# Performance work log

Measured on AMD Instinct MI355X. Metric: run time of the kernel, lower is better.

The kernel has to match this reference:

```python
import jax, jax.numpy as jnp
import numpy as np

NUM_HEADS = 8
NUM_POINTS = 4


def _bilinear_sample(value_hw, locs, H, W):
    """grid_sample(mode='bilinear', align_corners=False, padding_mode='zeros').
    value_hw: [B, heads, H*W, hd]; locs: [B, Nq, heads, P, 2] in [0,1].
    Returns [B, Nq, heads, P, hd]."""
    B, Nq, heads, P, _ = locs.shape
    hd = value_hw.shape[-1]
    # torch maps g in [-1,1] -> pixel ((g+1)*size-1)/2; with g = 2*loc-1 this is loc*size - 0.5
    x = locs[..., 0] * W - 0.5
    y = locs[..., 1] * H - 0.5
    x0 = jnp.floor(x); y0 = jnp.floor(y)
    wx = x - x0; wy = y - y0
    ix0 = x0.astype(jnp.int32); iy0 = y0.astype(jnp.int32)
    ix1 = ix0 + 1; iy1 = iy0 + 1

    def gather(iy, ix):
        valid = (ix >= 0) & (ix < W) & (iy >= 0) & (iy < H)
        flat = jnp.clip(iy, 0, H - 1) * W + jnp.clip(ix, 0, W - 1)  # [B,Nq,heads,P]
        flat_t = flat.transpose(0, 2, 1, 3).reshape(B, heads, Nq * P)
        v = jnp.take_along_axis(value_hw, flat_t[..., None], axis=2)  # [B,heads,Nq*P,hd]
        v = v.reshape(B, heads, Nq, P, hd).transpose(0, 2, 1, 3, 4)
        return v * valid[..., None].astype(v.dtype)

    out = (gather(iy0, ix0) * ((1 - wx) * (1 - wy))[..., None]
           + gather(iy0, ix1) * (wx * (1 - wy))[..., None]
           + gather(iy1, ix0) * ((1 - wx) * wy)[..., None]
           + gather(iy1, ix1) * (wx * wy)[..., None])
    return out


def setup_inputs() -> dict:
    key = jax.random.key(0)
    ks = jax.random.split(key, 12)
    B, Nq, C, H, W = 4, 8192, 256, 128, 128
    heads, P = NUM_HEADS, NUM_POINTS
    s = 1.0 / np.sqrt(C)
    return {
        "query": jax.random.normal(ks[0], (B, Nq, C), jnp.float32),
        "reference_points": jax.random.uniform(ks[1], (B, Nq, 2), jnp.float32),
        "value": jax.random.normal(ks[2], (B, H * W, C), jnp.float32),
        "W_off": jax.random.normal(ks[3], (C, heads * P * 2), jnp.float32) * s,
        "b_off": jax.random.normal(ks[4], (heads * P * 2,), jnp.float32) * 0.5,
        "W_attn": jax.random.normal(ks[5], (C, heads * P), jnp.float32) * s,
        "b_attn": jax.random.normal(ks[6], (heads * P,), jnp.float32) * 0.1,
        "W_v": jax.random.normal(ks[7], (C, C), jnp.float32) * s,
        "b_v": jax.random.normal(ks[8], (C,), jnp.float32) * 0.1,
        "W_out": jax.random.normal(ks[9], (C, C), jnp.float32) * s,
        "b_out": jax.random.normal(ks[10], (C,), jnp.float32) * 0.1,
        "H": H,
        "W": W,
    }


def reference(query, reference_points, value, W_off, b_off, W_attn, b_attn,
              W_v, b_v, W_out, b_out, H, W):
    B, Nq, C = query.shape
    heads, P = NUM_HEADS, NUM_POINTS
    hd = C // heads

    offsets = (query @ W_off + b_off).reshape(B, Nq, heads, P, 2)
    attn = jax.nn.softmax((query @ W_attn + b_attn).reshape(B, Nq, heads, P), axis=-1)

    off_x = offsets[..., 0] / float(W) * 0.1
    off_y = offsets[..., 1] / float(H) * 0.1
    locs = reference_points[:, :, None, None, :] + jnp.stack([off_x, off_y], axis=-1)
    locs = jnp.clip(locs, 0.0, 1.0)  # [B,Nq,heads,P,2]

    # value projection -> [B, heads, H*W, hd]
    v = (value @ W_v + b_v).reshape(B, H * W, heads, hd).transpose(0, 2, 1, 3)

    sampled = _bilinear_sample(v, locs, H, W)            # [B,Nq,heads,P,hd]
    agg = jnp.einsum('bnhp,bnhpd->bnhd', attn, sampled)  # weighted sum over points
    out = agg.reshape(B, Nq, C) @ W_out + b_out
    return out
```

## Files before the change

kernel.cpp:

```cpp
#include <hip/hip_runtime.h>
#include <cstdint>

#define NB 4
#define NQ 8192
#define NC 256
#define IH 128
#define IW 128
#define NHW (IH * IW)
#define NHEADS 8
#define NP 4
#define NHD 32

typedef __bf16 bf16x8 __attribute__((ext_vector_type(8)));
typedef float f32x4 __attribute__((ext_vector_type(4)));

union FragCast { uint4 q; bf16x8 v; };

__device__ __forceinline__ unsigned int f2bf(float f) {
    unsigned int u = __float_as_uint(f);
    return (u + 0x7FFFu + ((u >> 16) & 1u)) >> 16;
}
__device__ __forceinline__ float bf2f(unsigned short s) {
    return __uint_as_float(((unsigned int)s) << 16);
}

__global__ __launch_bounds__(256) void k_pack(
    const float* __restrict__ Wv, const float* __restrict__ Wout,
    const float* __restrict__ Woff, const float* __restrict__ Wattn,
    unsigned short* __restrict__ pkv, unsigned short* __restrict__ pko,
    unsigned short* __restrict__ pkq)
{
    const int tid = blockIdx.x * 256 + threadIdx.x;
    if (tid < 4096) {
        const float* src = (tid & 2048) ? Wout : Wv;
        unsigned short* dst = (tid & 2048) ? pko : pkv;
        const int rem = tid & 2047;
        const int kt = rem >> 8, col = rem & 255;
        unsigned short* d = dst + (size_t)(kt * 256 + col) * 32;
        const float* s = src + (size_t)kt * 32 * 256 + col;
#pragma unroll
        for (int j = 0; j < 32; ++j)
            d[j] = (unsigned short)f2bf(s[(size_t)j * 256]);
    } else {
        const int rem = tid - 4096;
        const int kt = rem / 96, col = rem % 96;
        unsigned short* d = pkq + (size_t)(kt * 96 + col) * 32;
        const float* s; int stride;
        if (col < 64) { s = Woff + col; stride = 64; }
        else          { s = Wattn + (col - 64); stride = 32; }
        s += (size_t)kt * 32 * stride;
#pragma unroll
        for (int j = 0; j < 32; ++j)
            d[j] = (unsigned short)f2bf(s[(size_t)j * stride]);
    }
}

#define VP_TPB 4
__global__ __launch_bounds__(512) void k_vproj(
    const float* __restrict__ value, const unsigned short* __restrict__ Bpk,
    const float* __restrict__ bv, unsigned short* __restrict__ vproj)
{
    const int t = threadIdx.x;
    const int l = t & 63, w = t >> 6;
    const int mh = w & 1, cg = w >> 1;

    __shared__ unsigned short A[2][64 * 256];

    uint4 bq[8][4];
#pragma unroll
    for (int kt = 0; kt < 8; ++kt)
#pragma unroll
        for (int i = 0; i < 4; ++i)
            bq[kt][i] = *reinterpret_cast<const uint4*>(
                Bpk + (size_t)kt * 8192 + (size_t)(cg * 4 + i) * 512 +
                (l & 15) * 32 + (l >> 4) * 8);

    float bb[4];
#pragma unroll
    for (int i = 0; i < 4; ++i) bb[i] = bv[cg * 64 + i * 16 + (l & 15)];

    const size_t tile0 = (size_t)blockIdx.x * VP_TPB;

    float4 st[8];
#pragma unroll
    for (int i = 0; i < 8; ++i) {
        const int chunk = i * 512 + t;
        const int row = chunk >> 6, k0 = (chunk & 63) * 4;
        st[i] = *reinterpret_cast<const float4*>(&value[(tile0 * 64 + row) * NC + k0]);
    }
#pragma unroll
    for (int i = 0; i < 8; ++i) {
        const int chunk = i * 512 + t;
        const int row = chunk >> 6, k0 = (chunk & 63) * 4;
        unsigned int byte = (unsigned int)(row * 512 + k0 * 2) ^ (unsigned int)((row & 7) << 4);
        *reinterpret_cast<uint2*>(reinterpret_cast<char*>(A[0]) + byte) =
            make_uint2(f2bf(st[i].x) | (f2bf(st[i].y) << 16),
                       f2bf(st[i].z) | (f2bf(st[i].w) << 16));
    }
    __syncthreads();

    for (int tt = 0; tt < VP_TPB; ++tt) {
        const int cur = tt & 1;
        if (tt + 1 < VP_TPB) {
#pragma unroll
            for (int i = 0; i < 8; ++i) {
                const int chunk = i * 512 + t;
                const int row = chunk >> 6, k0 = (chunk & 63) * 4;
                st[i] = *reinterpret_cast<const float4*>(
                    &value[((tile0 + tt + 1) * 64 + row) * NC + k0]);
            }
        }

        f32x4 acc[2][4];
#pragma unroll
        for (int m = 0; m < 2; ++m)
#pragma unroll
            for (int i = 0; i < 4; ++i) acc[m][i] = (f32x4)(bb[i]);

#pragma unroll
        for (int kt = 0; kt < 8; ++kt) {
#pragma unroll
            for (int m = 0; m < 2; ++m) {
                const int arow = mh * 32 + m * 16 + (l & 15);
                unsigned int abyte = (unsigned int)(arow * 512 + (kt * 32 + (l >> 4) * 8) * 2)
                                   ^ (unsigned int)((arow & 7) << 4);
                FragCast af;
                af.q = *reinterpret_cast<const uint4*>(reinterpret_cast<const char*>(A[cur]) + abyte);
#pragma unroll
                for (int i = 0; i < 4; ++i) {
                    FragCast bfc; bfc.q = bq[kt][i];
                    acc[m][i] = __builtin_amdgcn_mfma_f32_16x16x32_bf16(af.v, bfc.v, acc[m][i], 0, 0, 0);
                }
            }
        }

        const size_t rowbase = (tile0 + tt) * 64;
#pragma unroll
        for (int m = 0; m < 2; ++m)
#pragma unroll
            for (int i = 0; i < 4; ++i) {
                const int col = cg * 64 + i * 16 + (l & 15);
#pragma unroll
                for (int j = 0; j < 4; ++j) {
                    const size_t row = rowbase + mh * 32 + m * 16 + (l >> 4) * 4 + j;
                    vproj[row * NC + col] = (unsigned short)f2bf(acc[m][i][j]);
                }
            }

        if (tt + 1 < VP_TPB) {
#pragma unroll
            for (int i = 0; i < 8; ++i) {
                const int chunk = i * 512 + t;
                const int row = chunk >> 6, k0 = (chunk & 63) * 4;
                unsigned int byte = (unsigned int)(row * 512 + k0 * 2) ^ (unsigned int)((row & 7) << 4);
                *reinterpret_cast<uint2*>(reinterpret_cast<char*>(A[cur ^ 1]) + byte) =
                    make_uint2(f2bf(st[i].x) | (f2bf(st[i].y) << 16),
                               f2bf(st[i].z) | (f2bf(st[i].w) << 16));
            }
            __syncthreads();
        }
    }
}

__global__ __launch_bounds__(256) void k_fused(
    const float* __restrict__ query, const float* __restrict__ refp,
    const unsigned short* __restrict__ Bq, const float* __restrict__ boff,
    const float* __restrict__ battn, const unsigned short* __restrict__ vproj,
    const unsigned short* __restrict__ Bo, const float* __restrict__ bout,
    float* __restrict__ out)
{
    const int t = threadIdx.x;
    const int l = t & 63, w = t >> 6;
    const size_t q0 = (size_t)blockIdx.x * 16;
    const int b = (int)(q0 / NQ);

    __shared__ unsigned short A[16 * 256];
    __shared__ float locs_s[16][64];
    __shared__ float attn_s[16][32];
    __shared__ float refs[16][2];

#pragma unroll
    for (int i = 0; i < 4; ++i) {
        const int chunk = i * 256 + t;
        const int row = chunk >> 6, k0 = (chunk & 63) * 4;
        const float4 v4 = *reinterpret_cast<const float4*>(&query[(q0 + row) * NC + k0]);
        unsigned int byte = (unsigned int)(row * 512 + k0 * 2) ^ (unsigned int)((row & 7) << 4);
        *reinterpret_cast<uint2*>(reinterpret_cast<char*>(A) + byte) =
            make_uint2(f2bf(v4.x) | (f2bf(v4.y) << 16),
                       f2bf(v4.z) | (f2bf(v4.w) << 16));
    }
    if (t < 32) reinterpret_cast<float*>(refs)[t] = refp[q0 * 2 + t];
    __syncthreads();

    {
        const int arow = l & 15, achunk = l >> 4;
#pragma unroll
        for (int pass = 0; pass < 2; ++pass) {
            if (pass == 1 && w >= 2) break;
            const int ct = pass == 0 ? w : 4 + w;
            f32x4 acc = (f32x4)(0.f);
#pragma unroll
            for (int kt = 0; kt < 8; ++kt) {
                unsigned int abyte = (unsigned int)(arow * 512 + (kt * 32 + achunk * 8) * 2)
                                   ^ (unsigned int)((arow & 7) << 4);
                FragCast af;
                af.q = *reinterpret_cast<const uint4*>(reinterpret_cast<const char*>(A) + abyte);
                FragCast bfc;
                bfc.q = *reinterpret_cast<const uint4*>(
                    Bq + (size_t)kt * 3072 + (size_t)(ct * 16 + arow) * 32 + achunk * 8);
                acc = __builtin_amdgcn_mfma_f32_16x16x32_bf16(af.v, bfc.v, acc, 0, 0, 0);
            }
            const int col = ct * 16 + arow;
            if (col < 64) {
                const float bias = boff[col];
                const int xy = col & 1;
#pragma unroll
                for (int j = 0; j < 4; ++j) {
                    const int row = achunk * 4 + j;
                    float off = acc[j] + bias;
                    float loc = refs[row][xy] + off * (0.1f / 128.0f);
                    locs_s[row][col] = fminf(fmaxf(loc, 0.f), 1.f);
                }
            } else {
                const int lc = col - 64;
                const float bias = battn[lc];
#pragma unroll
                for (int j = 0; j < 4; ++j) {
                    const int row = achunk * 4 + j;
                    float v = acc[j] + bias;
                    float m = fmaxf(v, __shfl_xor(v, 1));
                    m = fmaxf(m, __shfl_xor(m, 2));
                    float e = __expf(v - m);
                    float s = e + __shfl_xor(e, 1);
                    s = s + __shfl_xor(s, 2);
                    attn_s[row][lc] = e / s;
                }
            }
        }
    }
    __syncthreads();

    {
        const int rhalf = l >> 5, h = (l >> 2) & 7, c = l & 3;
        const unsigned short* __restrict__ vb =
            vproj + (size_t)b * NHW * NC + h * NHD + c * 8;

#pragma unroll
        for (int it = 0; it < 2; ++it) {
            const int r = w * 4 + it * 2 + rhalf;
            float wts[16];
            uint4 vals[16];
#pragma unroll
            for (int p = 0; p < 4; ++p) {
                const float lx = locs_s[r][h * 8 + p * 2 + 0];
                const float ly = locs_s[r][h * 8 + p * 2 + 1];
                const float aw = attn_s[r][h * 4 + p];
                const float x = lx * (float)IW - 0.5f;
                const float y = ly * (float)IH - 0.5f;
                const float x0f = floorf(x), y0f = floorf(y);
                const float wx = x - x0f, wy = y - y0f;
                const int ix0 = (int)x0f, iy0 = (int)y0f;
                const int ix1 = ix0 + 1, iy1 = iy0 + 1;
                const int cx0 = max(ix0, 0), cy0 = max(iy0, 0);
                const int cx1 = min(ix1, IW - 1), cy1 = min(iy1, IH - 1);
                const float vx0 = (ix0 >= 0) ? 1.f : 0.f;
                const float vy0 = (iy0 >= 0) ? 1.f : 0.f;
                const float vx1 = (ix1 < IW) ? 1.f : 0.f;
                const float vy1 = (iy1 < IH) ? 1.f : 0.f;
                wts[p * 4 + 0] = aw * ((1.f - wx) * (1.f - wy) * vx0 * vy0);
                wts[p * 4 + 1] = aw * (wx * (1.f - wy) * vx1 * vy0);
                wts[p * 4 + 2] = aw * ((1.f - wx) * wy * vx0 * vy1);
                wts[p * 4 + 3] = aw * (wx * wy * vx1 * vy1);
                vals[p * 4 + 0] = *reinterpret_cast<const uint4*>(vb + (size_t)(cy0 * IW + cx0) * NC);
                vals[p * 4 + 1] = *reinterpret_cast<const uint4*>(vb + (size_t)(cy0 * IW + cx1) * NC);
                vals[p * 4 + 2] = *reinterpret_cast<const uint4*>(vb + (size_t)(cy1 * IW + cx0) * NC);
                vals[p * 4 + 3] = *reinterpret_cast<const uint4*>(vb + (size_t)(cy1 * IW + cx1) * NC);
            }
            __builtin_amdgcn_sched_barrier(0);
            float acc[8];
#pragma unroll
            for (int e = 0; e < 8; ++e) acc[e] = 0.f;
#pragma unroll
            for (int j = 0; j < 16; ++j) {
                const unsigned short* u = reinterpret_cast<const unsigned short*>(&vals[j]);
                const float wj = wts[j];
#pragma unroll
                for (int e = 0; e < 8; ++e) acc[e] = fmaf(wj, bf2f(u[e]), acc[e]);
            }
            uint4 pk;
            pk.x = f2bf(acc[0]) | (f2bf(acc[1]) << 16);
            pk.y = f2bf(acc[2]) | (f2bf(acc[3]) << 16);
            pk.z = f2bf(acc[4]) | (f2bf(acc[5]) << 16);
            pk.w = f2bf(acc[6]) | (f2bf(acc[7]) << 16);
            unsigned int byte = (unsigned int)(r * 512 + (h * NHD + c * 8) * 2)
                              ^ (unsigned int)((r & 7) << 4);
            *reinterpret_cast<uint4*>(reinterpret_cast<char*>(A) + byte) = pk;
        }
    }
    __syncthreads();

    {
        const int arow = l & 15, achunk = l >> 4;
        f32x4 acc2[4];
#pragma unroll
        for (int i = 0; i < 4; ++i) acc2[i] = (f32x4)(0.f);

#pragma unroll
        for (int kt = 0; kt < 8; ++kt) {
            unsigned int abyte = (unsigned int)(arow * 512 + (kt * 32 + achunk * 8) * 2)
                               ^ (unsigned int)((arow & 7) << 4);
            FragCast af;
            af.q = *reinterpret_cast<const uint4*>(reinterpret_cast<const char*>(A) + abyte);
            const unsigned short* bbase = Bo + (size_t)kt * 8192 + arow * 32 + achunk * 8;
#pragma unroll
            for (int i = 0; i < 4; ++i) {
                const int ct = w * 4 + i;
                FragCast bfc;
                bfc.q = *reinterpret_cast<const uint4*>(bbase + (size_t)ct * 512);
                acc2[i] = __builtin_amdgcn_mfma_f32_16x16x32_bf16(af.v, bfc.v, acc2[i], 0, 0, 0);
            }
        }

#pragma unroll
        for (int i = 0; i < 4; ++i) {
            const int col = (w * 4 + i) * 16 + arow;
            const float bbv = bout[col];
#pragma unroll
            for (int j = 0; j < 4; ++j) {
                const size_t row = q0 + achunk * 4 + j;
                out[row * NC + col] = acc2[i][j] + bbv;
            }
        }
    }
}

extern "C" void kernel_launch(void* const* d_in, const int* in_sizes, int n_in,
                              void* d_out, int out_size, void* d_ws, size_t ws_size,
                              hipStream_t stream) {
    const float* query = (const float*)d_in[0];
    const float* refp  = (const float*)d_in[1];
    const float* value = (const float*)d_in[2];
    const float* Woff  = (const float*)d_in[3];
    const float* boff  = (const float*)d_in[4];
    const float* Wattn = (const float*)d_in[5];
    const float* battn = (const float*)d_in[6];
    const float* Wv    = (const float*)d_in[7];
    const float* bv    = (const float*)d_in[8];
    const float* Wout  = (const float*)d_in[9];
    const float* bout  = (const float*)d_in[10];
    float* out = (float*)d_out;

    unsigned short* vproj  = (unsigned short*)d_ws;
    unsigned short* WvPk   = vproj + (size_t)NB * NHW * NC;
    unsigned short* WoutPk = WvPk + (size_t)NC * NC;
    unsigned short* WqPk   = WoutPk + (size_t)NC * NC;

    k_pack<<<dim3(19), dim3(256), 0, stream>>>(Wv, Wout, Woff, Wattn, WvPk, WoutPk, WqPk);
    k_vproj<<<dim3(256), dim3(512), 0, stream>>>(value, WvPk, bv, vproj);
    k_fused<<<dim3(NB * NQ / 16), dim3(256), 0, stream>>>(query, refp, WqPk, boff, battn,
                                                          vproj, WoutPk, bout, out);
}
```

Before: 74.13 us.

## Store value projection head-major and gather samples via global-to-LDS async loads

The projected value tensor is now written in a [B, heads, HW, hd] layout, so each head's 32-channel vector for a pixel occupies a contiguous 64 bytes. The bilinear gather no longer loads 16 uint4 values into registers. It issues global_load_lds into a per-wave LDS ring of 8 slots, waits with vmcnt, and reads the data back from LDS, overlapping the second batch of loads with the FMAs on the first. The goal is to cut register pressure, raise memory-level parallelism and improve locality of the random gathers. In exchange it adds 32KB of LDS per block, which may lower occupancy, and relies on hand-written waitcnt sequencing that is fragile.

New measurement: 79.60 us. 7.4% more time.

```diff
diff --git a/kernel.cpp b/kernel.cpp
--- a/kernel.cpp
+++ b/kernel.cpp
@@ -22,6 +22,11 @@
 }
 __device__ __forceinline__ float bf2f(unsigned short s) {
     return __uint_as_float(((unsigned int)s) << 16);
+}
+__device__ __forceinline__ void gld_lds16(const void* g, void* l) {
+    __builtin_amdgcn_global_load_lds(
+        (__attribute__((address_space(1))) const unsigned int*)g,
+        (__attribute__((address_space(3))) unsigned int*)l, 16, 0, 0);
 }
 
 __global__ __launch_bounds__(256) void k_pack(
@@ -140,10 +145,13 @@
 #pragma unroll
             for (int i = 0; i < 4; ++i) {
                 const int col = cg * 64 + i * 16 + (l & 15);
+                const int hh = col >> 5, dd = col & 31;
 #pragma unroll
                 for (int j = 0; j < 4; ++j) {
                     const size_t row = rowbase + mh * 32 + m * 16 + (l >> 4) * 4 + j;
-                    vproj[row * NC + col] = (unsigned short)f2bf(acc[m][i][j]);
+                    const size_t bidx = row >> 14, pix = row & (NHW - 1);
+                    vproj[(((bidx << 3) + hh) * (size_t)NHW + pix) * NHD + dd] =
+                        (unsigned short)f2bf(acc[m][i][j]);
                 }
             }
 
@@ -178,6 +186,7 @@
     __shared__ float locs_s[16][64];
     __shared__ float attn_s[16][32];
     __shared__ float refs[16][2];
+    __shared__ __align__(16) char gbuf[4][8][1024];
 
 #pragma unroll
     for (int i = 0; i < 4; ++i) {
@@ -242,14 +251,18 @@
 
     {
         const int rhalf = l >> 5, h = (l >> 2) & 7, c = l & 3;
-        const unsigned short* __restrict__ vb =
-            vproj + (size_t)b * NHW * NC + h * NHD + c * 8;
+        const char* __restrict__ vb =
+            reinterpret_cast<const char*>(vproj) + (size_t)b * NHEADS * NHW * (NHD * 2);
+        const unsigned int laneoff = (unsigned int)(h * NHW * 64 + c * 16);
+        char* gw = &gbuf[w][0][0];
+
+        asm volatile("s_waitcnt vmcnt(0)" ::: "memory");
 
 #pragma unroll
         for (int it = 0; it < 2; ++it) {
             const int r = w * 4 + it * 2 + rhalf;
             float wts[16];
-            uint4 vals[16];
+            unsigned int offs[16];
 #pragma unroll
             for (int p = 0; p < 4; ++p) {
                 const float lx = locs_s[r][h * 8 + p * 2 + 0];
@@ -271,22 +284,45 @@
                 wts[p * 4 + 1] = aw * (wx * (1.f - wy) * vx1 * vy0);
                 wts[p * 4 + 2] = aw * ((1.f - wx) * wy * vx0 * vy1);
                 wts[p * 4 + 3] = aw * (wx * wy * vx1 * vy1);
-                vals[p * 4 + 0] = *reinterpret_cast<const uint4*>(vb + (size_t)(cy0 * IW + cx0) * NC);
-                vals[p * 4 + 1] = *reinterpret_cast<const uint4*>(vb + (size_t)(cy0 * IW + cx1) * NC);
-                vals[p * 4 + 2] = *reinterpret_cast<const uint4*>(vb + (size_t)(cy1 * IW + cx0) * NC);
-                vals[p * 4 + 3] = *reinterpret_cast<const uint4*>(vb + (size_t)(cy1 * IW + cx1) * NC);
-            }
-            __builtin_amdgcn_sched_barrier(0);
+                offs[p * 4 + 0] = (unsigned int)(cy0 * IW + cx0) * 64u + laneoff;
+                offs[p * 4 + 1] = (unsigned int)(cy0 * IW + cx1) * 64u + laneoff;
+                offs[p * 4 + 2] = (unsigned int)(cy1 * IW + cx0) * 64u + laneoff;
+                offs[p * 4 + 3] = (unsigned int)(cy1 * IW + cx1) * 64u + laneoff;
+            }
+
             float acc[8];
 #pragma unroll
             for (int e = 0; e < 8; ++e) acc[e] = 0.f;
-#pragma unroll
-            for (int j = 0; j < 16; ++j) {
-                const unsigned short* u = reinterpret_cast<const unsigned short*>(&vals[j]);
-                const float wj = wts[j];
-#pragma unroll
-                for (int e = 0; e < 8; ++e) acc[e] = fmaf(wj, bf2f(u[e]), acc[e]);
-            }
+
+#pragma unroll
+            for (int j = 0; j < 8; ++j) gld_lds16(vb + offs[j], gw + j * 1024);
+
+#pragma unroll
+            for (int rd = 0; rd < 4; ++rd) {
+                if (rd < 2) { asm volatile("s_waitcnt vmcnt(4)" ::: "memory"); }
+                else if (rd == 2) { asm volatile("s_waitcnt vmcnt(4)" ::: "memory"); }
+                else { asm volatile("s_waitcnt vmcnt(0)" ::: "memory"); }
+                __builtin_amdgcn_sched_barrier(0);
+#pragma unroll
+                for (int jj = 0; jj < 4; ++jj) {
+                    const int j = rd * 4 + jj;
+                    const uint4 vq = *reinterpret_cast<const uint4*>(gw + (j & 7) * 1024 + (size_t)l * 16);
+                    const unsigned short* u = reinterpret_cast<const unsigned short*>(&vq);
+                    const float wj = wts[j];
+#pragma unroll
+                    for (int e = 0; e < 8; ++e) acc[e] = fmaf(wj, bf2f(u[e]), acc[e]);
+                }
+                if (rd < 2) {
+                    asm volatile("s_waitcnt lgkmcnt(0)" ::: "memory");
+                    __builtin_amdgcn_sched_barrier(0);
+#pragma unroll
+                    for (int jj = 0; jj < 4; ++jj) {
+                        const int j = 8 + rd * 4 + jj;
+                        gld_lds16(vb + offs[j], gw + (j & 7) * 1024);
+                    }
+                }
+            }
+
             uint4 pk;
             pk.x = f2bf(acc[0]) | (f2bf(acc[1]) << 16);
             pk.y = f2bf(acc[2]) | (f2bf(acc[3]) << 16);
@@ -295,6 +331,8 @@
             unsigned int byte = (unsigned int)(r * 512 + (h * NHD + c * 8) * 2)
                               ^ (unsigned int)((r & 7) << 4);
             *reinterpret_cast<uint4*>(reinterpret_cast<char*>(A) + byte) = pk;
+            asm volatile("s_waitcnt lgkmcnt(0)" ::: "memory");
+            __builtin_amdgcn_sched_barrier(0);
         }
     }
     __syncthreads();
```

## Double fused kernel block to 512 threads and repack weights into lane-contiguous fragments

Applied to the files above, without the earlier changes.

The fused sampling kernel now runs 512 threads per 16-query block, so each thread handles one query/head/chunk instead of two. The projection GEMMs spread over more waves (6 for the query projection, 2 column tiles per wave for the output projection). Packed weight layouts are changed so each lane's MFMA B-fragment is a contiguous 16-byte load at l*8, and gather offsets become 32-bit. This aims for more memory-level parallelism in the gathers and simpler weight loads, at the cost of larger blocks and possibly lower occupancy.

After: 68.09 us. -8.2%, faster.

```diff
diff --git a/kernel.cpp b/kernel.cpp
--- a/kernel.cpp
+++ b/kernel.cpp
@@ -36,22 +36,22 @@
         unsigned short* dst = (tid & 2048) ? pko : pkv;
         const int rem = tid & 2047;
         const int kt = rem >> 8, col = rem & 255;
-        unsigned short* d = dst + (size_t)(kt * 256 + col) * 32;
+        unsigned short* d = dst + (size_t)kt * 8192 + (col >> 4) * 512 + (col & 15) * 8;
         const float* s = src + (size_t)kt * 32 * 256 + col;
 #pragma unroll
         for (int j = 0; j < 32; ++j)
-            d[j] = (unsigned short)f2bf(s[(size_t)j * 256]);
+            d[(j >> 3) * 128 + (j & 7)] = (unsigned short)f2bf(s[(size_t)j * 256]);
     } else {
         const int rem = tid - 4096;
         const int kt = rem / 96, col = rem % 96;
-        unsigned short* d = pkq + (size_t)(kt * 96 + col) * 32;
+        unsigned short* d = pkq + (size_t)kt * 3072 + (col >> 4) * 512 + (col & 15) * 8;
         const float* s; int stride;
         if (col < 64) { s = Woff + col; stride = 64; }
         else          { s = Wattn + (col - 64); stride = 32; }
         s += (size_t)kt * 32 * stride;
 #pragma unroll
         for (int j = 0; j < 32; ++j)
-            d[j] = (unsigned short)f2bf(s[(size_t)j * stride]);
+            d[(j >> 3) * 128 + (j & 7)] = (unsigned short)f2bf(s[(size_t)j * stride]);
     }
 }
 
@@ -72,8 +72,7 @@
 #pragma unroll
         for (int i = 0; i < 4; ++i)
             bq[kt][i] = *reinterpret_cast<const uint4*>(
-                Bpk + (size_t)kt * 8192 + (size_t)(cg * 4 + i) * 512 +
-                (l & 15) * 32 + (l >> 4) * 8);
+                Bpk + (size_t)kt * 8192 + (size_t)(cg * 4 + i) * 512 + l * 8);
 
     float bb[4];
 #pragma unroll
@@ -162,7 +161,7 @@
     }
 }
 
-__global__ __launch_bounds__(256) void k_fused(
+__global__ __launch_bounds__(512) void k_fused(
     const float* __restrict__ query, const float* __restrict__ refp,
     const unsigned short* __restrict__ Bq, const float* __restrict__ boff,
     const float* __restrict__ battn, const unsigned short* __restrict__ vproj,
@@ -180,8 +179,8 @@
     __shared__ float refs[16][2];
 
 #pragma unroll
-    for (int i = 0; i < 4; ++i) {
-        const int chunk = i * 256 + t;
+    for (int i = 0; i < 2; ++i) {
+        const int chunk = i * 512 + t;
         const int row = chunk >> 6, k0 = (chunk & 63) * 4;
         const float4 v4 = *reinterpret_cast<const float4*>(&query[(q0 + row) * NC + k0]);
         unsigned int byte = (unsigned int)(row * 512 + k0 * 2) ^ (unsigned int)((row & 7) << 4);
@@ -192,138 +191,134 @@
     if (t < 32) reinterpret_cast<float*>(refs)[t] = refp[q0 * 2 + t];
     __syncthreads();
 
-    {
+    if (w < 6) {
         const int arow = l & 15, achunk = l >> 4;
-#pragma unroll
-        for (int pass = 0; pass < 2; ++pass) {
-            if (pass == 1 && w >= 2) break;
-            const int ct = pass == 0 ? w : 4 + w;
-            f32x4 acc = (f32x4)(0.f);
-#pragma unroll
-            for (int kt = 0; kt < 8; ++kt) {
-                unsigned int abyte = (unsigned int)(arow * 512 + (kt * 32 + achunk * 8) * 2)
-                                   ^ (unsigned int)((arow & 7) << 4);
-                FragCast af;
-                af.q = *reinterpret_cast<const uint4*>(reinterpret_cast<const char*>(A) + abyte);
-                FragCast bfc;
-                bfc.q = *reinterpret_cast<const uint4*>(
-                    Bq + (size_t)kt * 3072 + (size_t)(ct * 16 + arow) * 32 + achunk * 8);
-                acc = __builtin_amdgcn_mfma_f32_16x16x32_bf16(af.v, bfc.v, acc, 0, 0, 0);
-            }
-            const int col = ct * 16 + arow;
-            if (col < 64) {
-                const float bias = boff[col];
-                const int xy = col & 1;
-#pragma unroll
-                for (int j = 0; j < 4; ++j) {
-                    const int row = achunk * 4 + j;
-                    float off = acc[j] + bias;
-                    float loc = refs[row][xy] + off * (0.1f / 128.0f);
-                    locs_s[row][col] = fminf(fmaxf(loc, 0.f), 1.f);
-                }
-            } else {
-                const int lc = col - 64;
-                const float bias = battn[lc];
-#pragma unroll
-                for (int j = 0; j < 4; ++j) {
-                    const int row = achunk * 4 + j;
-                    float v = acc[j] + bias;
-                    float m = fmaxf(v, __shfl_xor(v, 1));
-                    m = fmaxf(m, __shfl_xor(m, 2));
-                    float e = __expf(v - m);
-                    float s = e + __shfl_xor(e, 1);
-                    s = s + __shfl_xor(s, 2);
-                    attn_s[row][lc] = e / s;
-                }
-            }
-        }
-    }
-    __syncthreads();
-
-    {
-        const int rhalf = l >> 5, h = (l >> 2) & 7, c = l & 3;
-        const unsigned short* __restrict__ vb =
-            vproj + (size_t)b * NHW * NC + h * NHD + c * 8;
-
-#pragma unroll
-        for (int it = 0; it < 2; ++it) {
-            const int r = w * 4 + it * 2 + rhalf;
-            float wts[16];
-            uint4 vals[16];
-#pragma unroll
-            for (int p = 0; p < 4; ++p) {
-                const float lx = locs_s[r][h * 8 + p * 2 + 0];
-                const float ly = locs_s[r][h * 8 + p * 2 + 1];
-                const float aw = attn_s[r][h * 4 + p];
-                const float x = lx * (float)IW - 0.5f;
-                const float y = ly * (float)IH - 0.5f;
-                const float x0f = floorf(x), y0f = floorf(y);
-                const float wx = x - x0f, wy = y - y0f;
-                const int ix0 = (int)x0f, iy0 = (int)y0f;
-                const int ix1 = ix0 + 1, iy1 = iy0 + 1;
-                const int cx0 = max(ix0, 0), cy0 = max(iy0, 0);
-                const int cx1 = min(ix1, IW - 1), cy1 = min(iy1, IH - 1);
-                const float vx0 = (ix0 >= 0) ? 1.f : 0.f;
-                const float vy0 = (iy0 >= 0) ? 1.f : 0.f;
-                const float vx1 = (ix1 < IW) ? 1.f : 0.f;
-                const float vy1 = (iy1 < IH) ? 1.f : 0.f;
-                wts[p * 4 + 0] = aw * ((1.f - wx) * (1.f - wy) * vx0 * vy0);
-                wts[p * 4 + 1] = aw * (wx * (1.f - wy) * vx1 * vy0);
-                wts[p * 4 + 2] = aw * ((1.f - wx) * wy * vx0 * vy1);
-                wts[p * 4 + 3] = aw * (wx * wy * vx1 * vy1);
-                vals[p * 4 + 0] = *reinterpret_cast<const uint4*>(vb + (size_t)(cy0 * IW + cx0) * NC);
-                vals[p * 4 + 1] = *reinterpret_cast<const uint4*>(vb + (size_t)(cy0 * IW + cx1) * NC);
-                vals[p * 4 + 2] = *reinterpret_cast<const uint4*>(vb + (size_t)(cy1 * IW + cx0) * NC);
-                vals[p * 4 + 3] = *reinterpret_cast<const uint4*>(vb + (size_t)(cy1 * IW + cx1) * NC);
-            }
-            __builtin_amdgcn_sched_barrier(0);
-            float acc[8];
-#pragma unroll
-            for (int e = 0; e < 8; ++e) acc[e] = 0.f;
-#pragma unroll
-            for (int j = 0; j < 16; ++j) {
-                const unsigned short* u = reinterpret_cast<const unsigned short*>(&vals[j]);
-                const float wj = wts[j];
-#pragma unroll
-                for (int e = 0; e < 8; ++e) acc[e] = fmaf(wj, bf2f(u[e]), acc[e]);
-            }
-            uint4 pk;
-            pk.x = f2bf(acc[0]) | (f2bf(acc[1]) << 16);
-            pk.y = f2bf(acc[2]) | (f2bf(acc[3]) << 16);
-            pk.z = f2bf(acc[4]) | (f2bf(acc[5]) << 16);
-            pk.w = f2bf(acc[6]) | (f2bf(acc[7]) << 16);
-            unsigned int byte = (unsigned int)(r * 512 + (h * NHD + c * 8) * 2)
-                              ^ (unsigned int)((r & 7) << 4);
-            *reinterpret_cast<uint4*>(reinterpret_cast<char*>(A) + byte) = pk;
-        }
-    }
-    __syncthreads();
-
-    {
-        const int arow = l & 15, achunk = l >> 4;
-        f32x4 acc2[4];
-#pragma unroll
-        for (int i = 0; i < 4; ++i) acc2[i] = (f32x4)(0.f);
-
+        f32x4 acc = (f32x4)(0.f);
 #pragma unroll
         for (int kt = 0; kt < 8; ++kt) {
             unsigned int abyte = (unsigned int)(arow * 512 + (kt * 32 + achunk * 8) * 2)
                                ^ (unsigned int)((arow & 7) << 4);
             FragCast af;
             af.q = *reinterpret_cast<const uint4*>(reinterpret_cast<const char*>(A) + abyte);
-            const unsigned short* bbase = Bo + (size_t)kt * 8192 + arow * 32 + achunk * 8;
-#pragma unroll
-            for (int i = 0; i < 4; ++i) {
-                const int ct = w * 4 + i;
+            FragCast bfc;
+            bfc.q = *reinterpret_cast<const uint4*>(Bq + (size_t)kt * 3072 + w * 512 + l * 8);
+            acc = __builtin_amdgcn_mfma_f32_16x16x32_bf16(af.v, bfc.v, acc, 0, 0, 0);
+        }
+        const int col = w * 16 + arow;
+        if (col < 64) {
+            const float bias = boff[col];
+            const int xy = col & 1;
+#pragma unroll
+            for (int j = 0; j < 4; ++j) {
+                const int row = achunk * 4 + j;
+                float off = acc[j] + bias;
+                float loc = refs[row][xy] + off * (0.1f / 128.0f);
+                locs_s[row][col] = fminf(fmaxf(loc, 0.f), 1.f);
+            }
+        } else {
+            const int lc = col - 64;
+            const float bias = battn[lc];
+#pragma unroll
+            for (int j = 0; j < 4; ++j) {
+                const int row = achunk * 4 + j;
+                float v = acc[j] + bias;
+                float m = fmaxf(v, __shfl_xor(v, 1));
+                m = fmaxf(m, __shfl_xor(m, 2));
+                float e = __expf(v - m);
+                float s = e + __shfl_xor(e, 1);
+                s = s + __shfl_xor(s, 2);
+                attn_s[row][lc] = e / s;
+            }
+        }
+    }
+    __syncthreads();
+
+    {
+        const int q = t >> 5, h = (t >> 2) & 7, c = t & 3;
+        const char* __restrict__ vb =
+            reinterpret_cast<const char*>(vproj) + (size_t)b * NHW * 512;
+        const unsigned int laneoff = (unsigned int)(h * 64 + c * 16);
+
+        float wts[16];
+        unsigned int offs[16];
+#pragma unroll
+        for (int p = 0; p < 4; ++p) {
+            const float lx = locs_s[q][h * 8 + p * 2 + 0];
+            const float ly = locs_s[q][h * 8 + p * 2 + 1];
+            const float aw = attn_s[q][h * 4 + p];
+            const float xx = lx * (float)IW - 0.5f;
+            const float yy = ly * (float)IH - 0.5f;
+            const float x0f = floorf(xx), y0f = floorf(yy);
+            const float wx = xx - x0f, wy = yy - y0f;
+            const int ix0 = (int)x0f, iy0 = (int)y0f;
+            const int ix1 = ix0 + 1, iy1 = iy0 + 1;
+            const int cx0 = max(ix0, 0), cy0 = max(iy0, 0);
+            const int cx1 = min(ix1, IW - 1), cy1 = min(iy1, IH - 1);
+            const float vx0 = (ix0 >= 0) ? 1.f : 0.f;
+            const float vy0 = (iy0 >= 0) ? 1.f : 0.f;
+            const float vx1 = (ix1 < IW) ? 1.f : 0.f;
+            const float vy1 = (iy1 < IH) ? 1.f : 0.f;
+            wts[p * 4 + 0] = aw * ((1.f - wx) * (1.f - wy) * vx0 * vy0);
+            wts[p * 4 + 1] = aw * (wx * (1.f - wy) * vx1 * vy0);
+            wts[p * 4 + 2] = aw * ((1.f - wx) * wy * vx0 * vy1);
+            wts[p * 4 + 3] = aw * (wx * wy * vx1 * vy1);
+            offs[p * 4 + 0] = (unsigned int)(cy0 * IW + cx0) * 512u + laneoff;
+            offs[p * 4 + 1] = (unsigned int)(cy0 * IW + cx1) * 512u + laneoff;
+            offs[p * 4 + 2] = (unsigned int)(cy1 * IW + cx0) * 512u + laneoff;
+            offs[p * 4 + 3] = (unsigned int)(cy1 * IW + cx1) * 512u + laneoff;
+        }
+
+        uint4 vals[16];
+#pragma unroll
+        for (int j = 0; j < 16; ++j)
+            vals[j] = *reinterpret_cast<const uint4*>(vb + offs[j]);
+
+        float acc[8];
+#pragma unroll
+        for (int e = 0; e < 8; ++e) acc[e] = 0.f;
+#pragma unroll
+        for (int j = 0; j < 16; ++j) {
+            const unsigned short* u = reinterpret_cast<const unsigned short*>(&vals[j]);
+            const float wj = wts[j];
+#pragma unroll
+            for (int e = 0; e < 8; ++e) acc[e] = fmaf(wj, bf2f(u[e]), acc[e]);
+        }
+
+        uint4 pk;
+        pk.x = f2bf(acc[0]) | (f2bf(acc[1]) << 16);
+        pk.y = f2bf(acc[2]) | (f2bf(acc[3]) << 16);
+        pk.z = f2bf(acc[4]) | (f2bf(acc[5]) << 16);
+        pk.w = f2bf(acc[6]) | (f2bf(acc[7]) << 16);
+        unsigned int byte = (unsigned int)(q * 512 + (h * NHD + c * 8) * 2)
+                          ^ (unsigned int)((q & 7) << 4);
+        *reinterpret_cast<uint4*>(reinterpret_cast<char*>(A) + byte) = pk;
+    }
+    __syncthreads();
+
+    {
+        const int arow = l & 15, achunk = l >> 4;
+        f32x4 acc2[2];
+#pragma unroll
+        for (int i = 0; i < 2; ++i) acc2[i] = (f32x4)(0.f);
+
+#pragma unroll
+        for (int kt = 0; kt < 8; ++kt) {
+            unsigned int abyte = (unsigned int)(arow * 512 + (kt * 32 + achunk * 8) * 2)
+                               ^ (unsigned int)((arow & 7) << 4);
+            FragCast af;
+            af.q = *reinterpret_cast<const uint4*>(reinterpret_cast<const char*>(A) + abyte);
+#pragma unroll
+            for (int i = 0; i < 2; ++i) {
+                const int ct = w * 2 + i;
                 FragCast bfc;
-                bfc.q = *reinterpret_cast<const uint4*>(bbase + (size_t)ct * 512);
+                bfc.q = *reinterpret_cast<const uint4*>(Bo + (size_t)kt * 8192 + ct * 512 + l * 8);
                 acc2[i] = __builtin_amdgcn_mfma_f32_16x16x32_bf16(af.v, bfc.v, acc2[i], 0, 0, 0);
             }
         }
 
 #pragma unroll
-        for (int i = 0; i < 4; ++i) {
-            const int col = (w * 4 + i) * 16 + arow;
+        for (int i = 0; i < 2; ++i) {
+            const int col = (w * 2 + i) * 16 + arow;
             const float bbv = bout[col];
 #pragma unroll
             for (int j = 0; j < 4; ++j) {
@@ -357,6 +352,6 @@
 
     k_pack<<<dim3(19), dim3(256), 0, stream>>>(Wv, Wout, Woff, Wattn, WvPk, WoutPk, WqPk);
     k_vproj<<<dim3(256), dim3(512), 0, stream>>>(value, WvPk, bv, vproj);
-    k_fused<<<dim3(NB * NQ / 16), dim3(256), 0, stream>>>(query, refp, WqPk, boff, battn,
+    k_fused<<<dim3(NB * NQ / 16), dim3(512), 0, stream>>>(query, refp, WqPk, boff, battn,
                                                           vproj, WoutPk, bout, out);
 }
```
